# Kernel tuning notes

Hardware: AMD Instinct MI355X
Metric: run time of the kernel (lower is better)

The kernel has to match this reference:

```python
import jax, jax.numpy as jnp
import numpy as np

SCALE = 0.08838834764831845  # 1/sqrt(head_dim=128)


def setup_inputs() -> dict:
    key = jax.random.key(0)
    ks = jax.random.split(key, 5)
    B, H, D = 16, 8, 128          # batch (decode seqs), kv heads, head_dim
    BS, BPS = 16, 128             # block_size, blocks per sequence
    NBLK = B * BPS                # total cache blocks (2048)
    CTX = 2048                    # context length per sequence
    q = jax.random.normal(ks[0], (B, H, D), jnp.float32)
    k = jax.random.normal(ks[1], (B, H, D), jnp.float32)
    v = jax.random.normal(ks[2], (B, H, D), jnp.float32)
    k_cache = jax.random.normal(ks[3], (NBLK, BS, H, D), jnp.float32)
    v_cache = jax.random.normal(ks[4], (NBLK, BS, H, D), jnp.float32)
    # each sequence owns a distinct contiguous set of blocks
    block_tables = jnp.arange(B * BPS, dtype=jnp.int32).reshape(B, BPS)
    context_lens = jnp.full((B,), CTX, dtype=jnp.int32)
    # slot for the newest token (position CTX-1) of each sequence
    last = CTX - 1
    slot_mapping = block_tables[:, last // BS] * BS + (last % BS)
    return {"q": q, "k": k, "v": v, "k_cache": k_cache, "v_cache": v_cache,
            "slot_mapping": slot_mapping.astype(jnp.int32),
            "block_tables": block_tables, "context_lens": context_lens}


def reference(q, k, v, k_cache, v_cache, slot_mapping, block_tables, context_lens):
    # ---- store_kvcache: scatter new k/v tokens into paged caches ----
    nblk, bs, H, D = k_cache.shape
    k_cache = k_cache.reshape(nblk * bs, H, D).at[slot_mapping].set(k).reshape(nblk, bs, H, D)
    v_cache = v_cache.reshape(nblk * bs, H, D).at[slot_mapping].set(v).reshape(nblk, bs, H, D)

    # ---- _sdpa_decode: paged gather + masked attention (q_per_seq = 1) ----
    B, nb = block_tables.shape
    T = nb * bs                              # max tokens per sequence
    token_idx = jnp.arange(T, dtype=jnp.int32)
    block_idx = token_idx // bs
    token_off = token_idx % bs
    block_ids = block_tables[:, block_idx]   # [B, T]
    k_all = k_cache[block_ids, token_off]    # [B, T, H, D]
    v_all = v_cache[block_ids, token_off]    # [B, T, H, D]

    valid = token_idx[None, :] < context_lens[:, None]           # [B, T]
    q_pos = context_lens - 1                                     # q_per_seq == 1
    causal = token_idx[None, :] <= q_pos[:, None]                # [B, T]
    mask = valid & causal

    scores = jnp.einsum("bhd,bthd->bht", q, k_all) * SCALE       # [B, H, T]
    scores = jnp.where(mask[:, None, :], scores, -jnp.inf)
    p = jax.nn.softmax(scores, axis=-1)
    out = jnp.einsum("bht,bthd->bhd", p, v_all)                  # [B, H, D]
    return out
```

## Files before the change

kernel.cpp:

```cpp
#include <hip/hip_runtime.h>
#include <math.h>

#define B_ 16
#define H_ 8
#define D_ 128
#define BS_ 16
#define BPS_ 128
#define T_ (BPS_ * BS_)
#define NSPLIT 8
#define CHUNK (T_ / NSPLIT)
#define SCALE_ 0.08838834764831845f

__global__ __launch_bounds__(256) void attn_partial(
    const float* __restrict__ q,
    const float* __restrict__ knew,
    const float* __restrict__ vnew,
    const float* __restrict__ kc,
    const float* __restrict__ vc,
    const int* __restrict__ btab,
    const int* __restrict__ clen,
    float* __restrict__ ws_m,
    float* __restrict__ ws_l,
    float* __restrict__ ws_o)
{
    const int c = blockIdx.x;
    const int h = blockIdx.y;
    const int b = blockIdx.z;
    const int tid = threadIdx.x;
    const int wave = tid >> 6;
    const int lane = tid & 63;
    const int hl = lane & 31;
    const int half = lane >> 5;
    const int ctx = clen[b];
    const int chunk_start = c * CHUNK;

    __shared__ float s_p[CHUNK];
    __shared__ float s_red[8];
    __shared__ float s_o[4][D_];
    __shared__ float s_ml[2];

    const float4 q4 = *(const float4*)(q + ((size_t)b * H_ + h) * D_ + 4 * hl);

    for (int it = 0; it < 32; ++it) {
        const int tl = wave * 64 + it * 2 + half;
        const int tg = chunk_start + tl;
        const int blk = btab[b * BPS_ + (tg >> 4)];
        const float* kp = (tg == ctx - 1)
            ? (knew + ((size_t)b * H_ + h) * D_)
            : (kc + (((size_t)blk * BS_ + (tg & 15)) * H_ + h) * D_);
        const float4 k4 = *(const float4*)(kp + 4 * hl);
        float s = q4.x * k4.x + q4.y * k4.y + q4.z * k4.z + q4.w * k4.w;
        s += __shfl_xor(s, 16);
        s += __shfl_xor(s, 8);
        s += __shfl_xor(s, 4);
        s += __shfl_xor(s, 2);
        s += __shfl_xor(s, 1);
        if (hl == 0) s_p[tl] = (tg < ctx) ? s * SCALE_ : -INFINITY;
    }
    __syncthreads();

    float sc = s_p[tid];
    float m = sc;
    m = fmaxf(m, __shfl_xor(m, 32));
    m = fmaxf(m, __shfl_xor(m, 16));
    m = fmaxf(m, __shfl_xor(m, 8));
    m = fmaxf(m, __shfl_xor(m, 4));
    m = fmaxf(m, __shfl_xor(m, 2));
    m = fmaxf(m, __shfl_xor(m, 1));
    if (lane == 0) s_red[wave] = m;
    __syncthreads();
    if (tid == 0) {
        float mm = fmaxf(fmaxf(s_red[0], s_red[1]), fmaxf(s_red[2], s_red[3]));
        s_ml[0] = fmaxf(mm, -1e30f);
    }
    __syncthreads();
    m = s_ml[0];

    float p = expf(sc - m);
    s_p[tid] = p;
    float l = p;
    l += __shfl_xor(l, 32);
    l += __shfl_xor(l, 16);
    l += __shfl_xor(l, 8);
    l += __shfl_xor(l, 4);
    l += __shfl_xor(l, 2);
    l += __shfl_xor(l, 1);
    if (lane == 0) s_red[4 + wave] = l;
    __syncthreads();
    if (tid == 0) s_ml[1] = s_red[4] + s_red[5] + s_red[6] + s_red[7];
    __syncthreads();

    float ox = 0.f, oy = 0.f;
    for (int it = 0; it < 64; ++it) {
        const int tl = wave * 64 + it;
        const int tg = chunk_start + tl;
        const float pw = s_p[tl];
        const int blk = btab[b * BPS_ + (tg >> 4)];
        const float* vp = (tg == ctx - 1)
            ? (vnew + ((size_t)b * H_ + h) * D_)
            : (vc + (((size_t)blk * BS_ + (tg & 15)) * H_ + h) * D_);
        const float2 v2 = *(const float2*)(vp + 2 * lane);
        ox += pw * v2.x;
        oy += pw * v2.y;
    }
    s_o[wave][2 * lane]     = ox;
    s_o[wave][2 * lane + 1] = oy;
    __syncthreads();

    const int idx = (b * H_ + h) * NSPLIT + c;
    if (tid < D_) {
        float oo = s_o[0][tid] + s_o[1][tid] + s_o[2][tid] + s_o[3][tid];
        ws_o[(size_t)idx * D_ + tid] = oo;
    }
    if (tid == 0) {
        ws_m[idx] = s_ml[0];
        ws_l[idx] = s_ml[1];
    }
}

__global__ __launch_bounds__(128) void attn_reduce(
    const float* __restrict__ ws_m,
    const float* __restrict__ ws_l,
    const float* __restrict__ ws_o,
    float* __restrict__ out)
{
    const int bh = blockIdx.x;
    const int d = threadIdx.x;

    float mm[NSPLIT];
    float m_g = -INFINITY;
    for (int c = 0; c < NSPLIT; ++c) {
        mm[c] = ws_m[bh * NSPLIT + c];
        m_g = fmaxf(m_g, mm[c]);
    }
    float l_g = 0.f, acc = 0.f;
    for (int c = 0; c < NSPLIT; ++c) {
        const float co = expf(mm[c] - m_g);
        l_g += ws_l[bh * NSPLIT + c] * co;
        acc += ws_o[(size_t)(bh * NSPLIT + c) * D_ + d] * co;
    }
    out[(size_t)bh * D_ + d] = acc / l_g;
}

extern "C" void kernel_launch(void* const* d_in, const int* in_sizes, int n_in,
                              void* d_out, int out_size, void* d_ws, size_t ws_size,
                              hipStream_t stream) {
    const float* q    = (const float*)d_in[0];
    const float* knew = (const float*)d_in[1];
    const float* vnew = (const float*)d_in[2];
    const float* kc   = (const float*)d_in[3];
    const float* vc   = (const float*)d_in[4];
    const int* btab = (const int*)d_in[6];
    const int* clen = (const int*)d_in[7];
    float* out = (float*)d_out;

    float* ws   = (float*)d_ws;
    float* ws_m = ws;
    float* ws_l = ws + B_ * H_ * NSPLIT;
    float* ws_o = ws + 2 * B_ * H_ * NSPLIT;

    dim3 grid1(NSPLIT, H_, B_);
    attn_partial<<<grid1, 256, 0, stream>>>(q, knew, vnew, kc, vc, btab, clen,
                                            ws_m, ws_l, ws_o);
    attn_reduce<<<dim3(B_ * H_), D_, 0, stream>>>(ws_m, ws_l, ws_o, out);
}
```

Baseline: 320.5 us.

## Double split count, batch K/V loads, cache block table in LDS

Raises the number of context splits from 8 to 16, doubling the grid to 2048 blocks so more of the GPU works on the memory-bound KV reads. Each thread now issues four independent float4 loads before using them, in both the score and PV passes. The PV pass switches from float2 to half-wave float4 loads, and block table entries are staged in shared memory. It also adds an occupancy hint, unrolls the loops and uses fast exp, at the cost of a larger reduction and fewer threads doing softmax work.

```diff
diff --git a/kernel.cpp b/kernel.cpp
--- a/kernel.cpp
+++ b/kernel.cpp
@@ -7,11 +7,12 @@
 #define BS_ 16
 #define BPS_ 128
 #define T_ (BPS_ * BS_)
-#define NSPLIT 8
+#define NSPLIT 16
 #define CHUNK (T_ / NSPLIT)
+#define NBLK_C (CHUNK / BS_)
 #define SCALE_ 0.08838834764831845f
 
-__global__ __launch_bounds__(256) void attn_partial(
+__global__ __launch_bounds__(256, 8) void attn_partial(
     const float* __restrict__ q,
     const float* __restrict__ knew,
     const float* __restrict__ vnew,
@@ -32,84 +33,112 @@
     const int hl = lane & 31;
     const int half = lane >> 5;
     const int ctx = clen[b];
-    const int chunk_start = c * CHUNK;
+    const int cs = c * CHUNK;
 
+    __shared__ int   s_bt[NBLK_C];
     __shared__ float s_p[CHUNK];
     __shared__ float s_red[8];
-    __shared__ float s_o[4][D_];
     __shared__ float s_ml[2];
+    __shared__ float s_o[8][D_];
 
-    const float4 q4 = *(const float4*)(q + ((size_t)b * H_ + h) * D_ + 4 * hl);
+    if (tid < NBLK_C) s_bt[tid] = btab[b * BPS_ + c * NBLK_C + tid];
 
-    for (int it = 0; it < 32; ++it) {
-        const int tl = wave * 64 + it * 2 + half;
-        const int tg = chunk_start + tl;
-        const int blk = btab[b * BPS_ + (tg >> 4)];
-        const float* kp = (tg == ctx - 1)
-            ? (knew + ((size_t)b * H_ + h) * D_)
-            : (kc + (((size_t)blk * BS_ + (tg & 15)) * H_ + h) * D_);
-        const float4 k4 = *(const float4*)(kp + 4 * hl);
-        float s = q4.x * k4.x + q4.y * k4.y + q4.z * k4.z + q4.w * k4.w;
-        s += __shfl_xor(s, 16);
-        s += __shfl_xor(s, 8);
-        s += __shfl_xor(s, 4);
-        s += __shfl_xor(s, 2);
-        s += __shfl_xor(s, 1);
-        if (hl == 0) s_p[tl] = (tg < ctx) ? s * SCALE_ : -INFINITY;
+    const float4 q4 = *(const float4*)(q + (size_t)(b * H_ + h) * D_ + 4 * hl);
+    __syncthreads();
+
+    #pragma unroll
+    for (int o = 0; o < 4; ++o) {
+        float4 k4[4];
+        int tls[4];
+        #pragma unroll
+        for (int j = 0; j < 4; ++j) {
+            const int tl = wave * 32 + o * 8 + j * 2 + half;
+            tls[j] = tl;
+            const int tg = cs + tl;
+            const int blk = s_bt[tl >> 4];
+            const float* kp = (tg == ctx - 1)
+                ? (knew + (size_t)(b * H_ + h) * D_)
+                : (kc + (((size_t)blk * BS_ + (tg & 15)) * H_ + h) * D_);
+            k4[j] = *(const float4*)(kp + 4 * hl);
+        }
+        #pragma unroll
+        for (int j = 0; j < 4; ++j) {
+            float s = q4.x * k4[j].x + q4.y * k4[j].y + q4.z * k4[j].z + q4.w * k4[j].w;
+            s += __shfl_xor(s, 16);
+            s += __shfl_xor(s, 8);
+            s += __shfl_xor(s, 4);
+            s += __shfl_xor(s, 2);
+            s += __shfl_xor(s, 1);
+            if (hl == 0) s_p[tls[j]] = (cs + tls[j] < ctx) ? s * SCALE_ : -INFINITY;
+        }
     }
     __syncthreads();
 
-    float sc = s_p[tid];
-    float m = sc;
-    m = fmaxf(m, __shfl_xor(m, 32));
-    m = fmaxf(m, __shfl_xor(m, 16));
-    m = fmaxf(m, __shfl_xor(m, 8));
-    m = fmaxf(m, __shfl_xor(m, 4));
-    m = fmaxf(m, __shfl_xor(m, 2));
-    m = fmaxf(m, __shfl_xor(m, 1));
-    if (lane == 0) s_red[wave] = m;
-    __syncthreads();
-    if (tid == 0) {
-        float mm = fmaxf(fmaxf(s_red[0], s_red[1]), fmaxf(s_red[2], s_red[3]));
-        s_ml[0] = fmaxf(mm, -1e30f);
+    float sc = 0.f;
+    if (tid < CHUNK) {
+        sc = s_p[tid];
+        float m = sc;
+        m = fmaxf(m, __shfl_xor(m, 32));
+        m = fmaxf(m, __shfl_xor(m, 16));
+        m = fmaxf(m, __shfl_xor(m, 8));
+        m = fmaxf(m, __shfl_xor(m, 4));
+        m = fmaxf(m, __shfl_xor(m, 2));
+        m = fmaxf(m, __shfl_xor(m, 1));
+        if (lane == 0) s_red[wave] = m;
     }
     __syncthreads();
-    m = s_ml[0];
+    if (tid == 0) s_ml[0] = fmaxf(fmaxf(s_red[0], s_red[1]), -1e30f);
+    __syncthreads();
+    const float m_c = s_ml[0];
 
-    float p = expf(sc - m);
-    s_p[tid] = p;
-    float l = p;
-    l += __shfl_xor(l, 32);
-    l += __shfl_xor(l, 16);
-    l += __shfl_xor(l, 8);
-    l += __shfl_xor(l, 4);
-    l += __shfl_xor(l, 2);
-    l += __shfl_xor(l, 1);
-    if (lane == 0) s_red[4 + wave] = l;
+    if (tid < CHUNK) {
+        const float p = __expf(sc - m_c);
+        s_p[tid] = p;
+        float l = p;
+        l += __shfl_xor(l, 32);
+        l += __shfl_xor(l, 16);
+        l += __shfl_xor(l, 8);
+        l += __shfl_xor(l, 4);
+        l += __shfl_xor(l, 2);
+        l += __shfl_xor(l, 1);
+        if (lane == 0) s_red[4 + wave] = l;
+    }
     __syncthreads();
-    if (tid == 0) s_ml[1] = s_red[4] + s_red[5] + s_red[6] + s_red[7];
+    if (tid == 0) s_ml[1] = s_red[4] + s_red[5];
     __syncthreads();
 
-    float ox = 0.f, oy = 0.f;
-    for (int it = 0; it < 64; ++it) {
-        const int tl = wave * 64 + it;
-        const int tg = chunk_start + tl;
-        const float pw = s_p[tl];
-        const int blk = btab[b * BPS_ + (tg >> 4)];
-        const float* vp = (tg == ctx - 1)
-            ? (vnew + ((size_t)b * H_ + h) * D_)
-            : (vc + (((size_t)blk * BS_ + (tg & 15)) * H_ + h) * D_);
-        const float2 v2 = *(const float2*)(vp + 2 * lane);
-        ox += pw * v2.x;
-        oy += pw * v2.y;
+    float4 acc = make_float4(0.f, 0.f, 0.f, 0.f);
+    #pragma unroll
+    for (int o = 0; o < 4; ++o) {
+        float4 v4[4];
+        float pw[4];
+        #pragma unroll
+        for (int j = 0; j < 4; ++j) {
+            const int tl = wave * 32 + o * 8 + j * 2 + half;
+            const int tg = cs + tl;
+            const int blk = s_bt[tl >> 4];
+            const float* vp = (tg == ctx - 1)
+                ? (vnew + (size_t)(b * H_ + h) * D_)
+                : (vc + (((size_t)blk * BS_ + (tg & 15)) * H_ + h) * D_);
+            v4[j] = *(const float4*)(vp + 4 * hl);
+            pw[j] = s_p[tl];
+        }
+        #pragma unroll
+        for (int j = 0; j < 4; ++j) {
+            acc.x += pw[j] * v4[j].x;
+            acc.y += pw[j] * v4[j].y;
+            acc.z += pw[j] * v4[j].z;
+            acc.w += pw[j] * v4[j].w;
+        }
     }
-    s_o[wave][2 * lane]     = ox;
-    s_o[wave][2 * lane + 1] = oy;
+    *(float4*)(&s_o[(wave << 1) | half][4 * hl]) = acc;
     __syncthreads();
 
     const int idx = (b * H_ + h) * NSPLIT + c;
     if (tid < D_) {
-        float oo = s_o[0][tid] + s_o[1][tid] + s_o[2][tid] + s_o[3][tid];
+        float oo = 0.f;
+        #pragma unroll
+        for (int r = 0; r < 8; ++r) oo += s_o[r][tid];
         ws_o[(size_t)idx * D_ + tid] = oo;
     }
     if (tid == 0) {
@@ -129,13 +158,15 @@
 
     float mm[NSPLIT];
     float m_g = -INFINITY;
+    #pragma unroll
     for (int c = 0; c < NSPLIT; ++c) {
         mm[c] = ws_m[bh * NSPLIT + c];
         m_g = fmaxf(m_g, mm[c]);
     }
     float l_g = 0.f, acc = 0.f;
+    #pragma unroll
     for (int c = 0; c < NSPLIT; ++c) {
-        const float co = expf(mm[c] - m_g);
+        const float co = __expf(mm[c] - m_g);
         l_g += ws_l[bh * NSPLIT + c] * co;
         acc += ws_o[(size_t)(bh * NSPLIT + c) * D_ + d] * co;
     }
```

After: 309.1 us. -3.6%, faster.
